# Kernel optimization log

Measured on AMD Instinct MI355X. Metric: run time of the kernel, lower is better.

## Reference

```python
import jax, jax.numpy as jnp
import numpy as np

N_NODES = 50000
N_EDGES = 1600000
IN_F, H_F, N_C = 128, 128, 16
NEG_SLOPE = 0.2  # DGL GATConv default


def setup_inputs() -> dict:
    key = jax.random.key(0)
    ks = jax.random.split(key, 12)
    def w(k, shape, fan_in):
        return jax.random.normal(k, shape, jnp.float32) / np.float32(np.sqrt(fan_in))
    return {
        "feat": jax.random.normal(ks[0], (N_NODES, IN_F), jnp.float32),
        "src": jax.random.randint(ks[1], (N_EDGES,), 0, N_NODES, dtype=jnp.int32),
        "dst": jax.random.randint(ks[2], (N_EDGES,), 0, N_NODES, dtype=jnp.int32),
        "W1": w(ks[3], (IN_F, H_F), IN_F), "al1": w(ks[4], (H_F,), H_F), "ar1": w(ks[5], (H_F,), H_F), "b1": jnp.zeros((H_F,), jnp.float32),
        "W2": w(ks[6], (H_F, H_F), H_F), "al2": w(ks[7], (H_F,), H_F), "ar2": w(ks[8], (H_F,), H_F), "b2": jnp.zeros((H_F,), jnp.float32),
        "W3": w(ks[9], (H_F, N_C), H_F), "al3": w(ks[10], (N_C,), N_C), "ar3": w(ks[11], (N_C,), N_C), "b3": jnp.zeros((N_C,), jnp.float32),
    }


def _gat_layer(h, src, dst, W, al, ar, b):
    # DGL GATConv (1 head): ft = W h; e_ij = LeakyReLU(a_l.ft_src + a_r.ft_dst);
    # alpha = edge_softmax over incoming edges of dst; out = sum alpha * ft_src + bias
    ft = h @ W                                   # [N, out]
    el = ft @ al                                 # [N]
    er = ft @ ar                                 # [N]
    e = jax.nn.leaky_relu(el[src] + er[dst], negative_slope=NEG_SLOPE)  # [E]
    emax = jax.ops.segment_max(e, dst, num_segments=N_NODES)
    emax = jnp.where(jnp.isfinite(emax), emax, 0.0)  # guard isolated nodes
    ex = jnp.exp(e - emax[dst])                  # [E]
    esum = jax.ops.segment_sum(ex, dst, num_segments=N_NODES)  # [N]
    agg = jax.ops.segment_sum(ex[:, None] * ft[src], dst, num_segments=N_NODES)  # [N, out]
    out = agg / jnp.where(esum > 0, esum, 1.0)[:, None] + b
    return jax.nn.relu(out)


def reference(feat, src, dst, W1, al1, ar1, b1, W2, al2, ar2, b2, W3, al3, ar3, b3):
    h = _gat_layer(feat, src, dst, W1, al1, ar1, b1)
    h = _gat_layer(h, src, dst, W2, al2, ar2, b2)
    h = _gat_layer(h, src, dst, W3, al3, ar3, b3)
    return h  # [N_NODES, N_C]
```

## Files before the change

### kernel.cpp

```cpp
#include <hip/hip_runtime.h>
#include <hip/hip_bf16.h>

#define NN 50000
#define NE 1600000
#define FF 128
#define CC 16
#define NB ((NN + 63) / 64)
#define NBLK 256
#define CH ((NE + NBLK - 1) / NBLK)

using bf16 = __hip_bfloat16;
using bf16x8 = __attribute__((ext_vector_type(8))) short;
using f32x4  = __attribute__((ext_vector_type(4))) float;

static __device__ __forceinline__ float ldf(const void* p, int i, int isbf){
    return isbf ? __bfloat162float(((const bf16*)p)[i]) : ((const float*)p)[i];
}
static __device__ __forceinline__ float bflo(unsigned u){
    union{unsigned x; float f;} c; c.x = u << 16; return c.f;
}
static __device__ __forceinline__ float bfhi(unsigned u){
    union{unsigned x; float f;} c; c.x = u & 0xFFFF0000u; return c.f;
}
static __device__ __forceinline__ float rdlanef(float v, int l){
    return __int_as_float(__builtin_amdgcn_readlane(__float_as_int(v), l));
}
static __device__ __forceinline__ unsigned short f2bfu(float v){
    bf16 b = __float2bfloat16(v);
    union{bf16 b; unsigned short u;} c; c.b = b; return c.u;
}

__global__ __launch_bounds__(256) void k_detect(const unsigned short* __restrict__ u,
                                                int* __restrict__ flag){
    int t = threadIdx.x;
    unsigned short lo = u[2 * t];
    int e = (lo >> 7) & 0xFF;
    int sane = (e >= 117 && e <= 137) ? 1 : 0;
    __shared__ int cnt;
    if (t == 0) cnt = 0;
    __syncthreads();
    atomicAdd(&cnt, sane);
    __syncthreads();
    if (t == 0) *flag = (cnt >= 128) ? 1 : 0;
}

__global__ __launch_bounds__(256) void k_zero(int* __restrict__ p, int n){
    int i = blockIdx.x * 256 + threadIdx.x;
    if (i < n) p[i] = 0;
}

__global__ __launch_bounds__(256) void k_wprep(const void* __restrict__ W1, const void* __restrict__ W2,
                                               const void* __restrict__ W3, const int* __restrict__ dflag,
                                               unsigned short* __restrict__ wtg){
    const int isbf = *dflag;
    int idx = blockIdx.x * 256 + threadIdx.x;
    if (idx < 32768){
        int l = idx >> 14;
        int e = idx & 16383;
        int f = e >> 7, k = e & 127;
        const void* W = l ? W2 : W1;
        wtg[idx] = f2bfu(ldf(W, k * FF + f, isbf));
    } else {
        int e = idx - 32768;
        int f = e >> 7, k = e & 127;
        wtg[idx] = f2bfu(ldf(W3, k * CC + f, isbf));
    }
}


__global__ __launch_bounds__(256) void k_bcount(const int* __restrict__ dst, int* __restrict__ bcounts,
                                                int* __restrict__ bh){
    __shared__ int hist[NB];
    const int t = threadIdx.x, b = blockIdx.x;
    for (int i = t; i < NB; i += 256) hist[i] = 0;
    __syncthreads();
    const int beg = b * CH, end = (beg + CH < NE) ? beg + CH : NE;
    for (int i = beg + t; i < end; i += 256){
        int d = dst[i];
        if ((unsigned)d >= NN) d = 0;
        atomicAdd(&hist[d >> 6], 1);
    }
    __syncthreads();
    for (int k = t; k < NB; k += 256){
        int v = hist[k];
        bh[k * NBLK + b] = v;
        if (v) atomicAdd(&bcounts[k], v);
    }
}

__global__ __launch_bounds__(256) void k_bscan(const int* __restrict__ bcounts, int* __restrict__ bbase,
                                               int* __restrict__ rowptr){
    __shared__ int s[256];
    const int t = threadIdx.x;
    constexpr int PT = (NB + 255) / 256;
    int loc[PT];
    int sum = 0;
    #pragma unroll
    for (int i = 0; i < PT; i++){
        int idx = t * PT + i;
        int v = (idx < NB) ? bcounts[idx] : 0;
        loc[i] = sum;
        sum += v;
    }
    s[t] = sum; __syncthreads();
    for (int off = 1; off < 256; off <<= 1){
        int x = (t >= off) ? s[t - off] : 0;
        __syncthreads();
        s[t] += x;
        __syncthreads();
    }
    int base = (t > 0) ? s[t - 1] : 0;
    #pragma unroll
    for (int i = 0; i < PT; i++){
        int idx = t * PT + i;
        if (idx < NB) bbase[idx] = base + loc[i];
    }
    if (t == 255){
        bbase[NB] = s[255];
        rowptr[NN] = s[255];
    }
}

__global__ __launch_bounds__(256) void k_boffset(const int* __restrict__ bbase, int* __restrict__ bh){
    int k = blockIdx.x * 4 + (threadIdx.x >> 6);
    int lane = threadIdx.x & 63;
    if (k >= NB) return;
    int v[4];
    int s = 0;
    #pragma unroll
    for (int i = 0; i < 4; i++){
        v[i] = bh[k * NBLK + 4 * lane + i];
        s += v[i];
    }
    int tot = s;
    #pragma unroll
    for (int off = 1; off < 64; off <<= 1){
        int x = __shfl_up(s, off);
        if (lane >= off) s += x;
    }
    int run = bbase[k] + s - tot;
    #pragma unroll
    for (int i = 0; i < 4; i++){
        bh[k * NBLK + 4 * lane + i] = run;
        run += v[i];
    }
}

__global__ __launch_bounds__(256) void k_bucket(const int* __restrict__ src, const int* __restrict__ dst,
                                                const int* __restrict__ bh, unsigned* __restrict__ bpairs){
    __shared__ int cur[NB];
    const int t = threadIdx.x, b = blockIdx.x;
    for (int k = t; k < NB; k += 256) cur[k] = bh[k * NBLK + b];
    __syncthreads();
    const int beg = b * CH, end = (beg + CH < NE) ? beg + CH : NE;
    for (int i = beg + t; i < end; i += 256){
        int s = src[i];
        int d = dst[i];
        if ((unsigned)s >= NN) s = 0;
        if ((unsigned)d >= NN) d = 0;
        int p = atomicAdd(&cur[d >> 6], 1);
        if ((unsigned)p < NE) bpairs[p] = (unsigned)s | ((unsigned)(d & 63) << 16);
    }
}

__global__ __launch_bounds__(256) void k_bsort(const unsigned* __restrict__ bpairs, const int* __restrict__ bbase,
                                               int* __restrict__ rowptr, int* __restrict__ csrsrc){
    __shared__ int cnt[64];
    __shared__ int cur[64];
    const int t = threadIdx.x;
    const int b = blockIdx.x;
    const int base = bbase[b];
    const int endb = bbase[b + 1];
    if (t < 64) cnt[t] = 0;
    __syncthreads();
    for (int i = base + t; i < endb; i += 256)
        atomicAdd(&cnt[bpairs[i] >> 16], 1);
    __syncthreads();
    if (t < 64){
        int v = cnt[t];
        int inc = v;
        #pragma unroll
        for (int off = 1; off < 64; off <<= 1){
            int x = __shfl_up(inc, off);
            if (t >= off) inc += x;
        }
        int excl = inc - v;
        cur[t] = excl;
        int d = b * 64 + t;
        if (d < NN) rowptr[d] = base + excl;
    }
    __syncthreads();
    for (int i = base + t; i < endb; i += 256){
        unsigned pr = bpairs[i];
        int p = atomicAdd(&cur[pr >> 16], 1);
        csrsrc[base + p] = (int)(pr & 0xFFFFu);
    }
}


#define XPAD 136

template<bool XDYN>
__global__ __launch_bounds__(256) void k_mgemm(const void* __restrict__ X, const unsigned short* __restrict__ wtg,
                                               const void* __restrict__ al, const void* __restrict__ ar,
                                               const int* __restrict__ dflag, bf16* __restrict__ ft,
                                               float* __restrict__ el, float* __restrict__ er){
    __shared__ unsigned short xs[64 * XPAD];
    __shared__ unsigned short wt[128 * XPAD];
    const int isbf = *dflag;
    const int t  = threadIdx.x;
    const int n0 = blockIdx.x * 64;

    for (int i2 = t; i2 < 8192; i2 += 256){
        unsigned v = ((const unsigned*)wtg)[i2];
        int r = i2 >> 6, c2 = (i2 & 63) * 2;
        *(unsigned*)&wt[r * XPAD + c2] = v;
    }
    for (int i2 = t; i2 < 4096; i2 += 256){
        int r = i2 >> 6, c2 = (i2 & 63) * 2;
        int n = n0 + r;
        float v0 = 0.f, v1 = 0.f;
        if (n < NN){
            if (XDYN){ v0 = ldf(X, n * FF + c2, isbf); v1 = ldf(X, n * FF + c2 + 1, isbf); }
            else     { v0 = ((const float*)X)[n * FF + c2]; v1 = ((const float*)X)[n * FF + c2 + 1]; }
        }
        unsigned pk = (unsigned)f2bfu(v0) | ((unsigned)f2bfu(v1) << 16);
        *(unsigned*)&xs[r * XPAD + c2] = pk;
    }
    __syncthreads();

    const int wv = t >> 6;
    const int lane = t & 63;
    const int quad = lane >> 4;
    const int mcol = lane & 15;

    bf16x8 afr[4];
    const unsigned short* xrow = &xs[(wv * 16 + mcol) * XPAD + quad * 8];
    #pragma unroll
    for (int kt = 0; kt < 4; kt++)
        afr[kt] = *(const bf16x8*)(xrow + kt * 32);

    float elp[4] = {0.f,0.f,0.f,0.f}, erp[4] = {0.f,0.f,0.f,0.f};

    #pragma unroll
    for (int f = 0; f < 8; f++){
        f32x4 acc = {0.f, 0.f, 0.f, 0.f};
        const unsigned short* wrow = &wt[(f * 16 + mcol) * XPAD + quad * 8];
        #pragma unroll
        for (int kt = 0; kt < 4; kt++){
            bf16x8 bfr = *(const bf16x8*)(wrow + kt * 32);
            acc = __builtin_amdgcn_mfma_f32_16x16x32_bf16(afr[kt], bfr, acc, 0, 0, 0);
        }
        int col = f * 16 + mcol;
        float alv = ldf(al, col, isbf);
        float arv = ldf(ar, col, isbf);
        #pragma unroll
        for (int reg = 0; reg < 4; reg++){
            int node = n0 + wv * 16 + quad * 4 + reg;
            float v = acc[reg];
            if (node < NN) ft[node * FF + col] = __float2bfloat16(v);
            elp[reg] += v * alv;
            erp[reg] += v * arv;
        }
    }

    #pragma unroll
    for (int reg = 0; reg < 4; reg++){
        float pl = elp[reg], pr = erp[reg];
        #pragma unroll
        for (int off = 1; off < 16; off <<= 1){
            pl += __shfl_xor(pl, off);
            pr += __shfl_xor(pr, off);
        }
        int node = n0 + wv * 16 + quad * 4 + reg;
        if (mcol == 0 && node < NN){ el[node] = pl; er[node] = pr; }
    }
}


__global__ __launch_bounds__(256) void k_mgemm3(const float* __restrict__ X, const unsigned short* __restrict__ wt3g,
                                                const void* __restrict__ al, const void* __restrict__ ar,
                                                const int* __restrict__ dflag, float* __restrict__ ft,
                                                float* __restrict__ el, float* __restrict__ er){
    __shared__ unsigned short xs[64 * XPAD];
    __shared__ unsigned short wt[16 * XPAD];
    const int isbf = *dflag;
    const int t  = threadIdx.x;
    const int n0 = blockIdx.x * 64;

    for (int i2 = t; i2 < 1024; i2 += 256){
        unsigned v = ((const unsigned*)wt3g)[i2];
        int r = i2 >> 6, c2 = (i2 & 63) * 2;
        *(unsigned*)&wt[r * XPAD + c2] = v;
    }
    for (int i2 = t; i2 < 4096; i2 += 256){
        int r = i2 >> 6, c2 = (i2 & 63) * 2;
        int n = n0 + r;
        float v0 = 0.f, v1 = 0.f;
        if (n < NN){
            v0 = X[n * FF + c2];
            v1 = X[n * FF + c2 + 1];
        }
        unsigned pk = (unsigned)f2bfu(v0) | ((unsigned)f2bfu(v1) << 16);
        *(unsigned*)&xs[r * XPAD + c2] = pk;
    }
    __syncthreads();

    const int wv = t >> 6;
    const int lane = t & 63;
    const int quad = lane >> 4;
    const int mcol = lane & 15;

    f32x4 acc = {0.f, 0.f, 0.f, 0.f};
    const unsigned short* xrow = &xs[(wv * 16 + mcol) * XPAD + quad * 8];
    const unsigned short* wrow = &wt[mcol * XPAD + quad * 8];
    #pragma unroll
    for (int kt = 0; kt < 4; kt++){
        bf16x8 afr = *(const bf16x8*)(xrow + kt * 32);
        bf16x8 bfr = *(const bf16x8*)(wrow + kt * 32);
        acc = __builtin_amdgcn_mfma_f32_16x16x32_bf16(afr, bfr, acc, 0, 0, 0);
    }

    float alv = ldf(al, mcol, isbf);
    float arv = ldf(ar, mcol, isbf);
    #pragma unroll
    for (int reg = 0; reg < 4; reg++){
        int node = n0 + wv * 16 + quad * 4 + reg;
        float v = acc[reg];
        if (node < NN) ft[node * CC + mcol] = v;
        float pl = v * alv, pr = v * arv;
        #pragma unroll
        for (int off = 1; off < 16; off <<= 1){
            pl += __shfl_xor(pl, off);
            pr += __shfl_xor(pr, off);
        }
        if (mcol == 0 && node < NN){ el[node] = pl; er[node] = pr; }
    }
}


__global__ __launch_bounds__(256) void k_agg128(const void* __restrict__ ftv, const float* __restrict__ el,
                                                const float* __restrict__ er, const int* __restrict__ rowptr,
                                                const int* __restrict__ csrsrc, const void* __restrict__ bias,
                                                const int* __restrict__ dflag, float* __restrict__ outp){
    const int isbf = *dflag;
    int lane = threadIdx.x & 63;
    int n = blockIdx.x * 4 + (threadIdx.x >> 6);
    if (n >= NN) return;
    int beg = rowptr[n], end = rowptr[n + 1];
    beg = (beg < 0) ? 0 : (beg > NE ? NE : beg);
    end = (end < beg) ? beg : (end > NE ? NE : end);
    int deg = end - beg;
    float erd = er[n];

    float m = -3.4e38f;
    int   s_c = 0;
    float e_c = 0.f;
    for (int i = beg + lane; i < end; i += 64){
        int s = csrsrc[i];
        if ((unsigned)s >= NN) s = 0;
        float e = el[s] + erd;
        e = (e >= 0.f) ? e : 0.2f * e;
        if (i < beg + 64){ s_c = s; e_c = e; }
        m = fmaxf(m, e);
    }
    #pragma unroll
    for (int off = 32; off; off >>= 1) m = fmaxf(m, __shfl_xor(m, off));

    int jmax = (deg < 64) ? deg : 64;
    float w_c = (lane < jmax) ? __expf(e_c - m) : 0.f;
    float lsum = w_c;
    #pragma unroll
    for (int off = 32; off; off >>= 1) lsum += __shfl_xor(lsum, off);

    const unsigned* ftb = (const unsigned*)ftv;
    float acc0 = 0.f, acc1 = 0.f;
    int j = 0;
    if (jmax >= 8){
        float w[8]; unsigned u[8];
        #pragma unroll
        for (int q = 0; q < 8; q++){
            int s = __builtin_amdgcn_readlane(s_c, q);
            w[q] = rdlanef(w_c, q);
            u[q] = (ftb + s * 64)[lane];
        }
        for (j = 8; j + 8 <= jmax; j += 8){
            float wn[8]; unsigned un[8];
            #pragma unroll
            for (int q = 0; q < 8; q++){
                int s = __builtin_amdgcn_readlane(s_c, j + q);
                wn[q] = rdlanef(w_c, j + q);
                un[q] = (ftb + s * 64)[lane];
            }
            #pragma unroll
            for (int q = 0; q < 8; q++){
                acc0 += w[q] * bflo(u[q]);
                acc1 += w[q] * bfhi(u[q]);
                w[q] = wn[q]; u[q] = un[q];
            }
        }
        #pragma unroll
        for (int q = 0; q < 8; q++){
            acc0 += w[q] * bflo(u[q]);
            acc1 += w[q] * bfhi(u[q]);
        }
    }
    for (; j < jmax; ++j){
        int s = __builtin_amdgcn_readlane(s_c, j);
        float w = rdlanef(w_c, j);
        unsigned u = (ftb + s * 64)[lane];
        acc0 += w * bflo(u); acc1 += w * bfhi(u);
    }
    for (int i = beg + 64; i < end; ++i){
        int s = csrsrc[i];
        if ((unsigned)s >= NN) s = 0;
        float e = el[s] + erd;
        e = (e >= 0.f) ? e : 0.2f * e;
        float w = __expf(e - m);
        unsigned u = (ftb + s * 64)[lane];
        lsum += w;
        acc0 += w * bflo(u); acc1 += w * bfhi(u);
    }
    float inv = 1.f / ((lsum > 0.f) ? lsum : 1.f);
    float2 o;
    o.x = fmaxf(acc0 * inv + ldf(bias, 2 * lane,     isbf), 0.f);
    o.y = fmaxf(acc1 * inv + ldf(bias, 2 * lane + 1, isbf), 0.f);
    ((float2*)outp)[n * 64 + lane] = o;
}


__global__ __launch_bounds__(256) void k_agg16(const float* __restrict__ ftv, const float* __restrict__ el,
                                               const float* __restrict__ er, const int* __restrict__ rowptr,
                                               const int* __restrict__ csrsrc, const void* __restrict__ bias,
                                               const int* __restrict__ dflag, void* __restrict__ outp){
    const int isbf = *dflag;
    int lane = threadIdx.x & 63;
    int n = blockIdx.x * 4 + (threadIdx.x >> 6);
    if (n >= NN) return;
    int beg = rowptr[n], end = rowptr[n + 1];
    beg = (beg < 0) ? 0 : (beg > NE ? NE : beg);
    end = (end < beg) ? beg : (end > NE ? NE : end);
    int deg = end - beg;
    float erd = er[n];

    float m = -3.4e38f;
    int   s_c = 0;
    float e_c = 0.f;
    for (int i = beg + lane; i < end; i += 64){
        int s = csrsrc[i];
        if ((unsigned)s >= NN) s = 0;
        float e = el[s] + erd;
        e = (e >= 0.f) ? e : 0.2f * e;
        if (i < beg + 64){ s_c = s; e_c = e; }
        m = fmaxf(m, e);
    }
    #pragma unroll
    for (int off = 32; off; off >>= 1) m = fmaxf(m, __shfl_xor(m, off));

    int jmax = (deg < 64) ? deg : 64;
    float w_c = (lane < jmax) ? __expf(e_c - m) : 0.f;
    float lsum = w_c;
    #pragma unroll
    for (int off = 32; off; off >>= 1) lsum += __shfl_xor(lsum, off);

    const float4* ftq = (const float4*)ftv;
    const int g   = lane >> 2;
    const int fl2 = lane & 3;
    int nbatch = (jmax + 15) >> 4;
    float wq[4]; float4 uq[4];
    #pragma unroll
    for (int q = 0; q < 4; q++){
        int eidx = (q * 16 + g) & 63;
        int s = __shfl(s_c, eidx);
        wq[q] = (q < nbatch) ? __shfl(w_c, eidx) : 0.f;
        uq[q] = ftq[(unsigned)s * 4 + fl2];
    }
    float a4[4] = {0.f,0.f,0.f,0.f};
    #pragma unroll
    for (int q = 0; q < 4; q++){
        a4[0] += wq[q] * uq[q].x;
        a4[1] += wq[q] * uq[q].y;
        a4[2] += wq[q] * uq[q].z;
        a4[3] += wq[q] * uq[q].w;
    }
    for (int i = beg + 64; i < end; ++i){
        int s = csrsrc[i];
        if ((unsigned)s >= NN) s = 0;
        float e = el[s] + erd;
        e = (e >= 0.f) ? e : 0.2f * e;
        float w = __expf(e - m);
        lsum += w;
        if (g == 0){
            float4 u = ftq[(unsigned)s * 4 + fl2];
            a4[0] += w * u.x; a4[1] += w * u.y; a4[2] += w * u.z; a4[3] += w * u.w;
        }
    }
    #pragma unroll
    for (int i = 0; i < 4; i++){
        a4[i] += __shfl_xor(a4[i], 4);
        a4[i] += __shfl_xor(a4[i], 8);
        a4[i] += __shfl_xor(a4[i], 16);
        a4[i] += __shfl_xor(a4[i], 32);
    }
    float inv = 1.f / ((lsum > 0.f) ? lsum : 1.f);
    if (lane < 4){
        float o0 = fmaxf(a4[0] * inv + ldf(bias, fl2 * 4 + 0, isbf), 0.f);
        float o1 = fmaxf(a4[1] * inv + ldf(bias, fl2 * 4 + 1, isbf), 0.f);
        float o2 = fmaxf(a4[2] * inv + ldf(bias, fl2 * 4 + 2, isbf), 0.f);
        float o3 = fmaxf(a4[3] * inv + ldf(bias, fl2 * 4 + 3, isbf), 0.f);
        if (isbf){
            uint2 pk;
            pk.x = (unsigned)f2bfu(o0) | ((unsigned)f2bfu(o1) << 16);
            pk.y = (unsigned)f2bfu(o2) | ((unsigned)f2bfu(o3) << 16);
            ((uint2*)outp)[n * 4 + fl2] = pk;
        } else {
            float4 o; o.x = o0; o.y = o1; o.z = o2; o.w = o3;
            ((float4*)outp)[n * 4 + fl2] = o;
        }
    }
}


static size_t align256(size_t x){ return (x + 255) & ~(size_t)255; }

extern "C" void kernel_launch(void* const* d_in, const int* in_sizes, int n_in,
                              void* d_out, int out_size, void* d_ws, size_t ws_size,
                              hipStream_t stream) {
    const void* feat = d_in[0];
    const int*  src  = (const int*)d_in[1];
    const int*  dst  = (const int*)d_in[2];
    const void* W1 = d_in[3];
    const void* al1= d_in[4];
    const void* ar1= d_in[5];
    const void* b1 = d_in[6];
    const void* W2 = d_in[7];
    const void* al2= d_in[8];
    const void* ar2= d_in[9];
    const void* b2 = d_in[10];
    const void* W3 = d_in[11];
    const void* al3= d_in[12];
    const void* ar3= d_in[13];
    const void* b3 = d_in[14];

    char* p = (char*)d_ws;
    size_t off = 0;
    auto carve = [&](size_t bytes)->void*{
        void* r = p + off;
        off += align256(bytes);
        return r;
    };
    float* ftA   = (float*)carve((size_t)NN * FF * 4);
    float* hB    = (float*)carve((size_t)NN * FF * 4);
    float* el    = (float*)carve((size_t)NN * 4);
    float* er    = (float*)carve((size_t)NN * 4);
    int*   rowptr= (int*)  carve((size_t)(NN + 1) * 4);
    int*   csrsrc= (int*)  carve((size_t)NE * 4);
    int*   bcounts=(int*)  carve((size_t)NB * 4);
    int*   bbase  =(int*)  carve((size_t)(NB + 1) * 4);
    int*   bh     =(int*)  carve((size_t)NB * NBLK * 4);
    unsigned short* wtg = (unsigned short*)carve((size_t)34816 * 2);
    int*   dflag  =(int*)  carve(256);
    unsigned* bpairs = (unsigned*)hB;
    void*  ftb   = ftA;
    (void)ws_size; (void)n_in; (void)in_sizes; (void)out_size;

    dim3 b256(256);

    k_detect<<<dim3(1), b256, 0, stream>>>((const unsigned short*)feat, dflag);
    k_wprep<<<dim3(136), b256, 0, stream>>>(W1, W2, W3, dflag, wtg);

    k_zero<<<dim3((NB + 255) / 256), b256, 0, stream>>>(bcounts, NB);
    k_bcount<<<dim3(NBLK), b256, 0, stream>>>(dst, bcounts, bh);
    k_bscan<<<dim3(1), b256, 0, stream>>>(bcounts, bbase, rowptr);
    k_boffset<<<dim3((NB + 3) / 4), b256, 0, stream>>>(bbase, bh);
    k_bucket<<<dim3(NBLK), b256, 0, stream>>>(src, dst, bh, bpairs);
    k_bsort<<<dim3(NB), b256, 0, stream>>>(bpairs, bbase, rowptr, csrsrc);

    const int mg_grid   = (NN + 63) / 64;
    const int node_grid = (NN + 3) / 4;

    k_mgemm<true><<<dim3(mg_grid), b256, 0, stream>>>(feat, wtg, al1, ar1, dflag, (bf16*)ftb, el, er);
    k_agg128<<<dim3(node_grid), b256, 0, stream>>>(ftb, el, er, rowptr, csrsrc, b1, dflag, hB);

    k_mgemm<false><<<dim3(mg_grid), b256, 0, stream>>>(hB, wtg + 16384, al2, ar2, dflag, (bf16*)ftb, el, er);
    k_agg128<<<dim3(node_grid), b256, 0, stream>>>(ftb, el, er, rowptr, csrsrc, b2, dflag, hB);

    k_mgemm3<<<dim3(mg_grid), b256, 0, stream>>>(hB, wtg + 32768, al3, ar3, dflag, (float*)ftb, el, er);
    k_agg16<<<dim3(node_grid), b256, 0, stream>>>((const float*)ftb, el, er, rowptr, csrsrc, b3, dflag, d_out);
}
```

Before: 340.4 us.

## Store intermediate layer activations as bf16 and merge prep kernels into one

The hidden activations written by the aggregation kernel are now packed to bf16 instead of fp32, and the next GEMM kernels load the packed words directly instead of converting from float. This halves intermediate activation traffic and removes per-element conversions in the GEMM staging loops. The format-detect, weight-prep and bucket-count zeroing kernels are merged into a single launch that recomputes the detection flag in every block. The trade-off is one extra bf16 rounding point on the layer outputs. The GEMM already cast its inputs to bf16, so the added rounding should make little numerical difference.

```diff
diff --git a/kernel.cpp b/kernel.cpp
--- a/kernel.cpp
+++ b/kernel.cpp
@@ -30,39 +30,31 @@
     union{bf16 b; unsigned short u;} c; c.b = b; return c.u;
 }
 
-__global__ __launch_bounds__(256) void k_detect(const unsigned short* __restrict__ u,
-                                                int* __restrict__ flag){
-    int t = threadIdx.x;
-    unsigned short lo = u[2 * t];
+__global__ __launch_bounds__(256) void k_prep(const unsigned short* __restrict__ featu,
+                                              const void* __restrict__ W1, const void* __restrict__ W2,
+                                              const void* __restrict__ W3, int* __restrict__ dflag,
+                                              int* __restrict__ bcounts, unsigned short* __restrict__ wtg){
+    __shared__ int cnt;
+    const int t = threadIdx.x;
+    if (t == 0) cnt = 0;
+    __syncthreads();
+    unsigned short lo = featu[2 * t];
     int e = (lo >> 7) & 0xFF;
-    int sane = (e >= 117 && e <= 137) ? 1 : 0;
-    __shared__ int cnt;
-    if (t == 0) cnt = 0;
-    __syncthreads();
-    atomicAdd(&cnt, sane);
-    __syncthreads();
-    if (t == 0) *flag = (cnt >= 128) ? 1 : 0;
-}
-
-__global__ __launch_bounds__(256) void k_zero(int* __restrict__ p, int n){
-    int i = blockIdx.x * 256 + threadIdx.x;
-    if (i < n) p[i] = 0;
-}
-
-__global__ __launch_bounds__(256) void k_wprep(const void* __restrict__ W1, const void* __restrict__ W2,
-                                               const void* __restrict__ W3, const int* __restrict__ dflag,
-                                               unsigned short* __restrict__ wtg){
-    const int isbf = *dflag;
-    int idx = blockIdx.x * 256 + threadIdx.x;
+    if (e >= 117 && e <= 137) atomicAdd(&cnt, 1);
+    __syncthreads();
+    const int isbf = (cnt >= 128) ? 1 : 0;
+    int idx = blockIdx.x * 256 + t;
+    if (idx == 0) *dflag = isbf;
+    if (idx < NB) bcounts[idx] = 0;
     if (idx < 32768){
         int l = idx >> 14;
-        int e = idx & 16383;
-        int f = e >> 7, k = e & 127;
+        int e2 = idx & 16383;
+        int f = e2 >> 7, k = e2 & 127;
         const void* W = l ? W2 : W1;
         wtg[idx] = f2bfu(ldf(W, k * FF + f, isbf));
-    } else {
-        int e = idx - 32768;
-        int f = e >> 7, k = e & 127;
+    } else if (idx < 34816){
+        int e2 = idx - 32768;
+        int f = e2 >> 7, k = e2 & 127;
         wtg[idx] = f2bfu(ldf(W3, k * CC + f, isbf));
     }
 }
@@ -219,12 +211,16 @@
     for (int i2 = t; i2 < 4096; i2 += 256){
         int r = i2 >> 6, c2 = (i2 & 63) * 2;
         int n = n0 + r;
-        float v0 = 0.f, v1 = 0.f;
+        unsigned pk = 0u;
         if (n < NN){
-            if (XDYN){ v0 = ldf(X, n * FF + c2, isbf); v1 = ldf(X, n * FF + c2 + 1, isbf); }
-            else     { v0 = ((const float*)X)[n * FF + c2]; v1 = ((const float*)X)[n * FF + c2 + 1]; }
-        }
-        unsigned pk = (unsigned)f2bfu(v0) | ((unsigned)f2bfu(v1) << 16);
+            if (XDYN){
+                float v0 = ldf(X, n * FF + c2, isbf);
+                float v1 = ldf(X, n * FF + c2 + 1, isbf);
+                pk = (unsigned)f2bfu(v0) | ((unsigned)f2bfu(v1) << 16);
+            } else {
+                pk = ((const unsigned*)X)[n * 64 + (i2 & 63)];
+            }
+        }
         *(unsigned*)&xs[r * XPAD + c2] = pk;
     }
     __syncthreads();
@@ -278,7 +274,7 @@
 }
 
 
-__global__ __launch_bounds__(256) void k_mgemm3(const float* __restrict__ X, const unsigned short* __restrict__ wt3g,
+__global__ __launch_bounds__(256) void k_mgemm3(const void* __restrict__ X, const unsigned short* __restrict__ wt3g,
                                                 const void* __restrict__ al, const void* __restrict__ ar,
                                                 const int* __restrict__ dflag, float* __restrict__ ft,
                                                 float* __restrict__ el, float* __restrict__ er){
@@ -296,12 +292,7 @@
     for (int i2 = t; i2 < 4096; i2 += 256){
         int r = i2 >> 6, c2 = (i2 & 63) * 2;
         int n = n0 + r;
-        float v0 = 0.f, v1 = 0.f;
-        if (n < NN){
-            v0 = X[n * FF + c2];
-            v1 = X[n * FF + c2 + 1];
-        }
-        unsigned pk = (unsigned)f2bfu(v0) | ((unsigned)f2bfu(v1) << 16);
+        unsigned pk = (n < NN) ? ((const unsigned*)X)[n * 64 + (i2 & 63)] : 0u;
         *(unsigned*)&xs[r * XPAD + c2] = pk;
     }
     __syncthreads();
@@ -342,7 +333,7 @@
 __global__ __launch_bounds__(256) void k_agg128(const void* __restrict__ ftv, const float* __restrict__ el,
                                                 const float* __restrict__ er, const int* __restrict__ rowptr,
                                                 const int* __restrict__ csrsrc, const void* __restrict__ bias,
-                                                const int* __restrict__ dflag, float* __restrict__ outp){
+                                                const int* __restrict__ dflag, unsigned* __restrict__ outp){
     const int isbf = *dflag;
     int lane = threadIdx.x & 63;
     int n = blockIdx.x * 4 + (threadIdx.x >> 6);
@@ -422,10 +413,10 @@
         acc0 += w * bflo(u); acc1 += w * bfhi(u);
     }
     float inv = 1.f / ((lsum > 0.f) ? lsum : 1.f);
-    float2 o;
-    o.x = fmaxf(acc0 * inv + ldf(bias, 2 * lane,     isbf), 0.f);
-    o.y = fmaxf(acc1 * inv + ldf(bias, 2 * lane + 1, isbf), 0.f);
-    ((float2*)outp)[n * 64 + lane] = o;
+    float o0 = fmaxf(acc0 * inv + ldf(bias, 2 * lane,     isbf), 0.f);
+    float o1 = fmaxf(acc1 * inv + ldf(bias, 2 * lane + 1, isbf), 0.f);
+    unsigned pk = (unsigned)f2bfu(o0) | ((unsigned)f2bfu(o1) << 16);
+    outp[n * 64 + lane] = pk;
 }
 
 
@@ -550,7 +541,7 @@
         return r;
     };
     float* ftA   = (float*)carve((size_t)NN * FF * 4);
-    float* hB    = (float*)carve((size_t)NN * FF * 4);
+    unsigned* hB = (unsigned*)carve((size_t)NN * FF * 4);
     float* el    = (float*)carve((size_t)NN * 4);
     float* er    = (float*)carve((size_t)NN * 4);
     int*   rowptr= (int*)  carve((size_t)(NN + 1) * 4);
@@ -566,10 +557,8 @@
 
     dim3 b256(256);
 
-    k_detect<<<dim3(1), b256, 0, stream>>>((const unsigned short*)feat, dflag);
-    k_wprep<<<dim3(136), b256, 0, stream>>>(W1, W2, W3, dflag, wtg);
-
-    k_zero<<<dim3((NB + 255) / 256), b256, 0, stream>>>(bcounts, NB);
+    k_prep<<<dim3(136), b256, 0, stream>>>((const unsigned short*)feat, W1, W2, W3, dflag, bcounts, wtg);
+
     k_bcount<<<dim3(NBLK), b256, 0, stream>>>(dst, bcounts, bh);
     k_bscan<<<dim3(1), b256, 0, stream>>>(bcounts, bbase, rowptr);
     k_boffset<<<dim3((NB + 3) / 4), b256, 0, stream>>>(bbase, bh);
```

After: 339.9 us. About the same (-0.1%).
